# Performance work log

Hardware: AMD Instinct MI355X
Metric: run time of the kernel (lower is better)

## Reference

```python
import jax, jax.numpy as jnp
import numpy as np

POOL = 3            # pool_size for this detection level
CENTER_TOP_NUM = 100
CENTER_THRES = 0.1
INST_THRES = 0.4


def _pool2d(x, op, k):
    """Stride-1 SAME pooling on NCHW, matching torch pad=(k-1)//2.
    avg matches torch avg_pool2d default count_include_pad=True (divide by k*k)."""
    if op == 'max':
        return jax.lax.reduce_window(x, -jnp.inf, jax.lax.max,
                                     (1, 1, k, k), (1, 1, 1, 1), 'SAME')
    s = jax.lax.reduce_window(x, 0.0, jax.lax.add,
                              (1, 1, k, k), (1, 1, 1, 1), 'SAME')
    return s / (k * k)


def setup_inputs() -> dict:
    key = jax.random.key(0)
    k1, k2, k3 = jax.random.split(key, 3)
    return {
        'thing_map':    jax.random.normal(k1, (1, 80, 128, 256), jnp.float32),
        'kernel_space': jax.random.normal(k2, (1, 256, 128, 256), jnp.float32),
        'embeddings':   jax.random.normal(k3, (1, 256, 256, 512), jnp.float32),
    }


def reference(thing_map, kernel_space, embeddings):
    B, C, H, W = thing_map.shape
    # --- peak detection (CenterNet-style) ---
    centers = jax.nn.sigmoid(thing_map)
    centers = (centers + _pool2d(centers, 'avg', POOL)) * 0.5
    fmap_max = _pool2d(centers, 'max', 3)
    peak_mask = (fmap_max == centers).astype(centers.dtype)
    centers = centers * peak_mask
    # --- topk over (class, h, w) ---
    K = min(H * W, CENTER_TOP_NUM // 2)  # 50
    flat = centers.reshape(B, C * H * W)
    scores, idx = jax.lax.top_k(flat, K)          # [B, K], sorted descending
    cats = idx // (H * W)                          # [B, K] class ids
    spatial = idx % (H * W)                        # [B, K] spatial index
    # masked_select(score > thres) replaced by a static-shape validity mask
    valid = (scores > CENTER_THRES).astype(scores.dtype)
    # --- sample kernels at peak locations ---
    D = kernel_space.shape[1]
    kflat = kernel_space.reshape(B, D, H * W)      # batch dims (h w)
    kernels = jnp.take_along_axis(kflat, spatial[:, None, :], axis=2)  # [B, D, K]
    kernels = kernels.transpose(0, 2, 1)           # [B, K, D]
    # --- maskifier: dynamic conv of kernels over embeddings, then sigmoid ---
    thing_masks = jax.nn.sigmoid(
        jnp.einsum('bkd,bdhw->bkhw', kernels, embeddings))  # [B, K, He, We]
    # --- mask-based score rescoring ---
    binm = (thing_masks > INST_THRES).astype(thing_masks.dtype)
    score_factor = (thing_masks * binm).sum((-2, -1))
    score_factor = score_factor / jnp.maximum(binm.sum((-2, -1)), 1e-8)
    scores = scores * score_factor * valid
    return thing_masks, scores, cats
```

## Files before the change

kernel.cpp:

```cpp
#include <hip/hip_runtime.h>
#include <hip/hip_bf16.h>
#include <math.h>


constexpr int C   = 80;
constexpr int H   = 128;
constexpr int W   = 256;
constexpr int HW  = H * W;
constexpr int CHW = C * HW;
constexpr int D   = 256;
constexpr int NPIX = 256 * 512;
constexpr int K   = 50;
constexpr int KP  = 52;
constexpr int NBINS = 4096;
constexpr int MAXCAND = 8192;
constexpr int SEL_CAP = 4096;
constexpr int MASK_ELEMS = K * NPIX;

constexpr int CAP = CHW / 4;

constexpr int OFF_PKVAL  = 0;
constexpr int OFF_PKIDX  = CAP;
constexpr int OFF_HIST   = 2 * CAP;
constexpr int OFF_CUTBIN = OFF_HIST + NBINS;
constexpr int OFF_PCOUNT = OFF_CUTBIN + 1;
constexpr int OFF_CCOUNT = OFF_PCOUNT + 1;
constexpr int OFF_FNUM   = OFF_CCOUNT + 1;
constexpr int OFF_FDEN   = OFF_FNUM + K;
constexpr int OFF_CVAL   = OFF_FDEN + K;
constexpr int OFF_CIDX   = OFF_CVAL + MAXCAND;
constexpr int OFF_TSCORE = OFF_CIDX + MAXCAND;
constexpr int OFF_TSPAT  = OFF_TSCORE + K;
constexpr int OFF_TCAT   = OFF_TSPAT + K;
constexpr int OFF_A      = (OFF_TCAT + K + 3) & ~3;
constexpr int WS_END     = OFF_A + KP * D;
constexpr int ZERO_WORDS = NBINS + 3 + 2 * K;

#define REP13(X) X(0) X(1) X(2) X(3) X(4) X(5) X(6) X(7) X(8) X(9) X(10) X(11) X(12)

__device__ __forceinline__ float sigmoidf(float x) {
    return 1.0f / (1.0f + expf(-x));
}

__device__ __forceinline__ int value_bin(float v) {
    int b = (int)(v * (float)NBINS);
    return b > NBINS - 1 ? NBINS - 1 : b;
}

constexpr int TW = 64, TH = 4;
constexpr int SW = TW + 4, SH = TH + 4;
constexpr int CW = TW + 2, CH2 = TH + 2;

__global__ __launch_bounds__(256) void peaks_kernel(
        const float* __restrict__ x, float* __restrict__ ws) {
    __shared__ float ssig[SH][SW];
    __shared__ float scen[CH2][CW];
    __shared__ int   shist[NBINS];
    __shared__ int   wcnt[4];
    __shared__ int   bbase;

    const int tid = threadIdx.x;
    for (int i = tid; i < NBINS; i += 256) shist[i] = 0;

    const int b  = blockIdx.x;
    const int c  = b >> 7;
    const int t  = b & 127;
    const int h0 = (t >> 2) * TH;
    const int w0 = (t & 3) * TW;
    const float* xc = x + c * HW;

    for (int l = tid; l < SH * SW; l += 256) {
        int r = l / SW, q = l - r * SW;
        int h = h0 + r - 2, w = w0 + q - 2;
        float s = 0.0f;
        if ((unsigned)h < (unsigned)H && (unsigned)w < (unsigned)W)
            s = sigmoidf(xc[(h << 8) + w]);
        ssig[r][q] = s;
    }
    __syncthreads();

    for (int l = tid; l < CH2 * CW; l += 256) {
        int r = l / CW, q = l - r * CW;
        int h = h0 + r - 1, w = w0 + q - 1;
        float cv = -INFINITY;
        if ((unsigned)h < (unsigned)H && (unsigned)w < (unsigned)W) {
            float s0 = ssig[r + 1][q + 1];
            float sum = 0.0f;
            #pragma unroll
            for (int dh = 0; dh < 3; dh++)
                #pragma unroll
                for (int dw = 0; dw < 3; dw++)
                    sum += ssig[r + dh][q + dw];
            cv = 0.5f * (s0 + sum / 9.0f);
        }
        scen[r][q] = cv;
    }
    __syncthreads();

    const int dw = tid & 63, dh = tid >> 6;
    float c0 = scen[dh + 1][dw + 1];
    float m = c0;
    #pragma unroll
    for (int i = 0; i < 3; i++)
        #pragma unroll
        for (int j = 0; j < 3; j++)
            m = fmaxf(m, scen[dh + i][dw + j]);
    const bool peak = (c0 == m);
    const int idx = c * HW + ((h0 + dh) << 8) + (w0 + dw);

    if (peak) atomicAdd(&shist[value_bin(c0)], 1);

    unsigned long long mk = __ballot(peak);
    const int lane = tid & 63, wv = tid >> 6;
    if (lane == 0) wcnt[wv] = __popcll(mk);
    __syncthreads();
    if (tid == 0) {
        int e0 = wcnt[0], e1 = wcnt[1], e2 = wcnt[2], e3 = wcnt[3];
        wcnt[0] = 0; wcnt[1] = e0; wcnt[2] = e0 + e1; wcnt[3] = e0 + e1 + e2;
        bbase = atomicAdd((int*)ws + OFF_PCOUNT, e0 + e1 + e2 + e3);
    }
    __syncthreads();
    if (peak) {
        int pos = bbase + wcnt[wv] + __popcll(mk & ((1ull << lane) - 1ull));
        if (pos < CAP) {
            ws[OFF_PKVAL + pos] = c0;
            ((int*)ws)[OFF_PKIDX + pos] = idx;
        }
    }

    __syncthreads();
    for (int i = tid; i < NBINS; i += 256) {
        int v = shist[i];
        if (v) atomicAdd((int*)ws + OFF_HIST + i, v);
    }
}

__global__ void scan_kernel(float* ws) {
    __shared__ int chunk[256];
    const int* hist = (const int*)ws + OFF_HIST;
    int t = threadIdx.x;
    int s = 0;
    #pragma unroll
    for (int b = t * 16; b < t * 16 + 16; b++) s += hist[b];
    chunk[t] = s;
    __syncthreads();
    if (t == 0) {
        int cum = 0, cutbin = 0;
        bool found = false;
        for (int ch = 255; ch >= 0 && !found; ch--) {
            if (cum + chunk[ch] >= K) {
                for (int b = ch * 16 + 15; b >= ch * 16; b--) {
                    cum += hist[b];
                    if (cum >= K) { cutbin = b; found = true; break; }
                }
            } else {
                cum += chunk[ch];
            }
        }
        ((int*)ws)[OFF_CUTBIN] = found ? cutbin : 0;
    }
}

__global__ void gather_kernel(float* ws) {
    int q = blockIdx.x * 256 + threadIdx.x;
    int n = ((const int*)ws)[OFF_PCOUNT];
    if (n > CAP) n = CAP;
    if (q >= n) return;
    float v = ws[OFF_PKVAL + q];
    int cutbin = ((const int*)ws)[OFF_CUTBIN];
    if (value_bin(v) >= cutbin) {
        int pos = atomicAdd((int*)ws + OFF_CCOUNT, 1);
        if (pos < MAXCAND) {
            ws[OFF_CVAL + pos] = v;
            ((int*)ws)[OFF_CIDX + pos] = ((const int*)ws)[OFF_PKIDX + q];
        }
    }
}

__global__ void select_kernel(float* ws) {
    __shared__ float sv[SEL_CAP];
    __shared__ int   si[SEL_CAP];
    __shared__ unsigned smask[MAXCAND / 32];
    const float* cval = ws + OFF_CVAL;
    const int*   cidx = (const int*)ws + OFF_CIDX;
    int n = ((const int*)ws)[OFF_CCOUNT];
    if (n > MAXCAND) n = MAXCAND;
    int t = threadIdx.x;

    int cap = n < SEL_CAP ? n : SEL_CAP;
    for (int q = t; q < cap; q += 64) { sv[q] = cval[q]; si[q] = cidx[q]; }
    for (int q = t; q < MAXCAND / 32; q += 64) smask[q] = 0u;
    __syncthreads();

    for (int j = 0; j < K; j++) {
        float bv = -1e30f; int bi = 0x7fffffff; int bp = -1;
        for (int q = t; q < n; q += 64) {
            if (smask[q >> 5] & (1u << (q & 31))) continue;
            float v; int id;
            if (q < SEL_CAP) { v = sv[q]; id = si[q]; }
            else             { v = cval[q]; id = cidx[q]; }
            if (v > bv || (v == bv && id < bi)) { bv = v; bi = id; bp = q; }
        }
        #pragma unroll
        for (int m = 1; m < 64; m <<= 1) {
            float ov = __shfl_xor(bv, m);
            int   oi = __shfl_xor(bi, m);
            int   op = __shfl_xor(bp, m);
            if (ov > bv || (ov == bv && oi < bi)) { bv = ov; bi = oi; bp = op; }
        }
        if (t == 0) {
            float score = (bp >= 0) ? bv : 0.0f;
            int   idx   = (bp >= 0) ? bi : 0;
            ws[OFF_TSCORE + j] = score;
            ((int*)ws)[OFF_TSPAT + j] = idx & (HW - 1);
            ((int*)ws)[OFF_TCAT + j]  = idx >> 15;
            if (bp >= 0) smask[bp >> 5] |= (1u << (bp & 31));
        }
        __syncthreads();
    }
}

__global__ void gatherA_kernel(const float* __restrict__ ksp, float* __restrict__ ws) {
    int k = blockIdx.x;
    int d = threadIdx.x;
    float v = 0.0f;
    if (k < K) {
        int sp = ((const int*)ws)[OFF_TSPAT + k];
        v = ksp[d * HW + sp];
    }
    ws[OFF_A + d * KP + k] = v;
}

#define FMAROW(i) { const float4 a_ = Arow[i]; \
    c##i.x = fmaf(e, a_.x, c##i.x); \
    c##i.y = fmaf(e, a_.y, c##i.y); \
    c##i.z = fmaf(e, a_.z, c##i.z); \
    c##i.w = fmaf(e, a_.w, c##i.w); }

__global__ __launch_bounds__(256) void gemm_kernel(
        const float* __restrict__ emb,
        const float* __restrict__ At,
        float* __restrict__ out) {
    const int n = blockIdx.x * 256 + threadIdx.x;
    const float4* __restrict__ Af = (const float4*)At;

#define DECLC(i) float4 c##i = make_float4(0.0f, 0.0f, 0.0f, 0.0f);
    REP13(DECLC)
#undef DECLC

    const float* __restrict__ ep = emb + n;
    float cur0 = ep[(size_t)0 * NPIX];
    float cur1 = ep[(size_t)1 * NPIX];
    float cur2 = ep[(size_t)2 * NPIX];
    float cur3 = ep[(size_t)3 * NPIX];

    for (int d = 0; d < D - 4; d += 4) {
        const float* q = ep + (size_t)(d + 4) * NPIX;
        float nxt0 = q[0];
        float nxt1 = q[(size_t)1 * NPIX];
        float nxt2 = q[(size_t)2 * NPIX];
        float nxt3 = q[(size_t)3 * NPIX];
        { const float4* Arow = Af + (d + 0) * 13; const float e = cur0; REP13(FMAROW) }
        { const float4* Arow = Af + (d + 1) * 13; const float e = cur1; REP13(FMAROW) }
        { const float4* Arow = Af + (d + 2) * 13; const float e = cur2; REP13(FMAROW) }
        { const float4* Arow = Af + (d + 3) * 13; const float e = cur3; REP13(FMAROW) }
        cur0 = nxt0; cur1 = nxt1; cur2 = nxt2; cur3 = nxt3;
    }
    { const float4* Arow = Af + (D - 4) * 13; const float e = cur0; REP13(FMAROW) }
    { const float4* Arow = Af + (D - 3) * 13; const float e = cur1; REP13(FMAROW) }
    { const float4* Arow = Af + (D - 2) * 13; const float e = cur2; REP13(FMAROW) }
    { const float4* Arow = Af + (D - 1) * 13; const float e = cur3; REP13(FMAROW) }

    float* op = out + n;
#define EPI(i) \
    if (4*(i)+0 < K) op[(size_t)(4*(i)+0) * NPIX] = 1.0f/(1.0f+expf(-c##i.x)); \
    if (4*(i)+1 < K) op[(size_t)(4*(i)+1) * NPIX] = 1.0f/(1.0f+expf(-c##i.y)); \
    if (4*(i)+2 < K) op[(size_t)(4*(i)+2) * NPIX] = 1.0f/(1.0f+expf(-c##i.z)); \
    if (4*(i)+3 < K) op[(size_t)(4*(i)+3) * NPIX] = 1.0f/(1.0f+expf(-c##i.w));
    REP13(EPI)
#undef EPI
}

__global__ __launch_bounds__(256) void rescore_kernel(
        const float* __restrict__ masks,
        float* __restrict__ fnum,
        float* __restrict__ fden) {
    const int k = blockIdx.x;
    const float4* mk = (const float4*)(masks + (size_t)k * NPIX);
    float a = 0.0f; float b = 0.0f;
    int base = blockIdx.y * 2048 + threadIdx.x;
    #pragma unroll
    for (int r = 0; r < 8; r++) {
        float4 v = mk[base + r * 256];
        if (v.x > 0.4f) { a += v.x; b += 1.0f; }
        if (v.y > 0.4f) { a += v.y; b += 1.0f; }
        if (v.z > 0.4f) { a += v.z; b += 1.0f; }
        if (v.w > 0.4f) { a += v.w; b += 1.0f; }
    }
    a += __shfl_xor(a, 1);  b += __shfl_xor(b, 1);
    a += __shfl_xor(a, 2);  b += __shfl_xor(b, 2);
    a += __shfl_xor(a, 4);  b += __shfl_xor(b, 4);
    a += __shfl_xor(a, 8);  b += __shfl_xor(b, 8);
    a += __shfl_xor(a, 16); b += __shfl_xor(b, 16);
    a += __shfl_xor(a, 32); b += __shfl_xor(b, 32);
    __shared__ float sa[4], sb[4];
    int wave = threadIdx.x >> 6;
    if ((threadIdx.x & 63) == 0) { sa[wave] = a; sb[wave] = b; }
    __syncthreads();
    if (threadIdx.x == 0) {
        atomicAdd(&fnum[k], sa[0] + sa[1] + sa[2] + sa[3]);
        atomicAdd(&fden[k], sb[0] + sb[1] + sb[2] + sb[3]);
    }
}

__global__ void finalize_kernel(const float* __restrict__ ws, float* __restrict__ out) {
    int j = threadIdx.x;
    if (j < K) {
        float s = ws[OFF_TSCORE + j];
        float num = ws[OFF_FNUM + j];
        float den = ws[OFF_FDEN + j];
        float factor = num / fmaxf(den, 1e-8f);
        float valid = (s > 0.1f) ? 1.0f : 0.0f;
        out[MASK_ELEMS + j]     = s * factor * valid;
        out[MASK_ELEMS + K + j] = (float)(((const int*)ws)[OFF_TCAT + j]);
    }
}

extern "C" void kernel_launch(void* const* d_in, const int* in_sizes, int n_in,
                              void* d_out, int out_size, void* d_ws, size_t ws_size,
                              hipStream_t stream) {
    const float* thing_map = (const float*)d_in[0];
    const float* ksp       = (const float*)d_in[1];
    const float* emb       = (const float*)d_in[2];
    float* out = (float*)d_out;
    float* ws  = (float*)d_ws;

    hipMemsetAsync(ws + OFF_HIST, 0, (size_t)ZERO_WORDS * 4, stream);

    peaks_kernel<<<C * 128, 256, 0, stream>>>(thing_map, ws);
    scan_kernel<<<1, 256, 0, stream>>>(ws);
    gather_kernel<<<CAP / 256, 256, 0, stream>>>(ws);
    select_kernel<<<1, 64, 0, stream>>>(ws);
    gatherA_kernel<<<KP, D, 0, stream>>>(ksp, ws);
    gemm_kernel<<<NPIX / 256, 256, 0, stream>>>(emb, ws + OFF_A, out);
    rescore_kernel<<<dim3(K, 16), 256, 0, stream>>>(out, ws + OFF_FNUM, ws + OFF_FDEN);
    finalize_kernel<<<1, 64, 0, stream>>>(ws, out);
}
```

Baseline: 446.3 us.

## Replace shared histogram and global atomic compaction with replicated global histograms and per-block slots

The peaks kernel no longer keeps a 4096-bin shared-memory histogram that it clears and flushes per block. It now does direct global atomics into one of 16 replicated histograms, which the scan kernel sums. Peak compaction drops the global atomic counter and one barrier in favour of fixed 64-slot regions per block with a per-block count that the gather kernel reads. This removes LDS initialisation, the flush loop and a serialising atomic, at the cost of more scattered global atomics and a larger, sparser peak buffer.

Result: faster. 376.8 us (-15.6%).

```diff
diff --git a/kernel.cpp b/kernel.cpp
--- a/kernel.cpp
+++ b/kernel.cpp
@@ -13,18 +13,21 @@
 constexpr int K   = 50;
 constexpr int KP  = 52;
 constexpr int NBINS = 4096;
+constexpr int NREP  = 16;
 constexpr int MAXCAND = 8192;
 constexpr int SEL_CAP = 4096;
 constexpr int MASK_ELEMS = K * NPIX;
 
-constexpr int CAP = CHW / 4;
+constexpr int NBLK  = C * 128;
+constexpr int SLOTS = 64;
+constexpr int CAP   = NBLK * SLOTS;
 
 constexpr int OFF_PKVAL  = 0;
 constexpr int OFF_PKIDX  = CAP;
-constexpr int OFF_HIST   = 2 * CAP;
-constexpr int OFF_CUTBIN = OFF_HIST + NBINS;
-constexpr int OFF_PCOUNT = OFF_CUTBIN + 1;
-constexpr int OFF_CCOUNT = OFF_PCOUNT + 1;
+constexpr int OFF_PKCNT  = 2 * CAP;
+constexpr int OFF_HIST   = OFF_PKCNT + NBLK;
+constexpr int OFF_CUTBIN = OFF_HIST + NREP * NBINS;
+constexpr int OFF_CCOUNT = OFF_CUTBIN + 1;
 constexpr int OFF_FNUM   = OFF_CCOUNT + 1;
 constexpr int OFF_FDEN   = OFF_FNUM + K;
 constexpr int OFF_CVAL   = OFF_FDEN + K;
@@ -33,8 +36,7 @@
 constexpr int OFF_TSPAT  = OFF_TSCORE + K;
 constexpr int OFF_TCAT   = OFF_TSPAT + K;
 constexpr int OFF_A      = (OFF_TCAT + K + 3) & ~3;
-constexpr int WS_END     = OFF_A + KP * D;
-constexpr int ZERO_WORDS = NBINS + 3 + 2 * K;
+constexpr int ZERO_WORDS = NREP * NBINS + 2 + 2 * K;
 
 #define REP13(X) X(0) X(1) X(2) X(3) X(4) X(5) X(6) X(7) X(8) X(9) X(10) X(11) X(12)
 
@@ -55,13 +57,9 @@
         const float* __restrict__ x, float* __restrict__ ws) {
     __shared__ float ssig[SH][SW];
     __shared__ float scen[CH2][CW];
-    __shared__ int   shist[NBINS];
     __shared__ int   wcnt[4];
-    __shared__ int   bbase;
 
     const int tid = threadIdx.x;
-    for (int i = tid; i < NBINS; i += 256) shist[i] = 0;
-
     const int b  = blockIdx.x;
     const int c  = b >> 7;
     const int t  = b & 127;
@@ -108,40 +106,45 @@
     const bool peak = (c0 == m);
     const int idx = c * HW + ((h0 + dh) << 8) + (w0 + dw);
 
-    if (peak) atomicAdd(&shist[value_bin(c0)], 1);
+    if (peak) {
+        atomicAdd((int*)ws + OFF_HIST + (b & (NREP - 1)) * NBINS + value_bin(c0), 1);
+    }
 
     unsigned long long mk = __ballot(peak);
     const int lane = tid & 63, wv = tid >> 6;
     if (lane == 0) wcnt[wv] = __popcll(mk);
     __syncthreads();
+    int woff = 0;
+    #pragma unroll
+    for (int i = 0; i < 4; i++) if (i < wv) woff += wcnt[i];
+    if (peak) {
+        int rank = woff + __popcll(mk & ((1ull << lane) - 1ull));
+        if (rank < SLOTS) {
+            ws[OFF_PKVAL + b * SLOTS + rank] = c0;
+            ((int*)ws)[OFF_PKIDX + b * SLOTS + rank] = idx;
+        }
+    }
     if (tid == 0) {
-        int e0 = wcnt[0], e1 = wcnt[1], e2 = wcnt[2], e3 = wcnt[3];
-        wcnt[0] = 0; wcnt[1] = e0; wcnt[2] = e0 + e1; wcnt[3] = e0 + e1 + e2;
-        bbase = atomicAdd((int*)ws + OFF_PCOUNT, e0 + e1 + e2 + e3);
-    }
-    __syncthreads();
-    if (peak) {
-        int pos = bbase + wcnt[wv] + __popcll(mk & ((1ull << lane) - 1ull));
-        if (pos < CAP) {
-            ws[OFF_PKVAL + pos] = c0;
-            ((int*)ws)[OFF_PKIDX + pos] = idx;
-        }
-    }
-
-    __syncthreads();
-    for (int i = tid; i < NBINS; i += 256) {
-        int v = shist[i];
-        if (v) atomicAdd((int*)ws + OFF_HIST + i, v);
+        int total = wcnt[0] + wcnt[1] + wcnt[2] + wcnt[3];
+        ((int*)ws)[OFF_PKCNT + b] = total > SLOTS ? SLOTS : total;
     }
 }
 
 __global__ void scan_kernel(float* ws) {
+    __shared__ int shist[NBINS];
     __shared__ int chunk[256];
     const int* hist = (const int*)ws + OFF_HIST;
     int t = threadIdx.x;
+    for (int b = t; b < NBINS; b += 256) {
+        int s = 0;
+        #pragma unroll
+        for (int r = 0; r < NREP; r++) s += hist[r * NBINS + b];
+        shist[b] = s;
+    }
+    __syncthreads();
     int s = 0;
     #pragma unroll
-    for (int b = t * 16; b < t * 16 + 16; b++) s += hist[b];
+    for (int b = t * 16; b < t * 16 + 16; b++) s += shist[b];
     chunk[t] = s;
     __syncthreads();
     if (t == 0) {
@@ -150,7 +153,7 @@
         for (int ch = 255; ch >= 0 && !found; ch--) {
             if (cum + chunk[ch] >= K) {
                 for (int b = ch * 16 + 15; b >= ch * 16; b--) {
-                    cum += hist[b];
+                    cum += shist[b];
                     if (cum >= K) { cutbin = b; found = true; break; }
                 }
             } else {
@@ -163,16 +166,18 @@
 
 __global__ void gather_kernel(float* ws) {
     int q = blockIdx.x * 256 + threadIdx.x;
-    int n = ((const int*)ws)[OFF_PCOUNT];
-    if (n > CAP) n = CAP;
-    if (q >= n) return;
-    float v = ws[OFF_PKVAL + q];
-    int cutbin = ((const int*)ws)[OFF_CUTBIN];
-    if (value_bin(v) >= cutbin) {
-        int pos = atomicAdd((int*)ws + OFF_CCOUNT, 1);
-        if (pos < MAXCAND) {
-            ws[OFF_CVAL + pos] = v;
-            ((int*)ws)[OFF_CIDX + pos] = ((const int*)ws)[OFF_PKIDX + q];
+    int bid = q >> 6;
+    int i = q & 63;
+    int cnt = ((const int*)ws)[OFF_PKCNT + bid];
+    if (i < cnt) {
+        float v = ws[OFF_PKVAL + q];
+        int cutbin = ((const int*)ws)[OFF_CUTBIN];
+        if (value_bin(v) >= cutbin) {
+            int pos = atomicAdd((int*)ws + OFF_CCOUNT, 1);
+            if (pos < MAXCAND) {
+                ws[OFF_CVAL + pos] = v;
+                ((int*)ws)[OFF_CIDX + pos] = ((const int*)ws)[OFF_PKIDX + q];
+            }
         }
     }
 }
@@ -337,7 +342,7 @@
 
     hipMemsetAsync(ws + OFF_HIST, 0, (size_t)ZERO_WORDS * 4, stream);
 
-    peaks_kernel<<<C * 128, 256, 0, stream>>>(thing_map, ws);
+    peaks_kernel<<<NBLK, 256, 0, stream>>>(thing_map, ws);
     scan_kernel<<<1, 256, 0, stream>>>(ws);
     gather_kernel<<<CAP / 256, 256, 0, stream>>>(ws);
     select_kernel<<<1, 64, 0, stream>>>(ws);
```
